# Optimization experiments

Measured on AMD Instinct MI355X. Metric: run time of the kernel, lower is better.

## Reference

```python
import jax, jax.numpy as jnp
import numpy as np

N = 50000       # nodes
D_IN = 256      # in_channels
D_OUT = 256     # out_channels
E1 = 300000     # edges for TAGConv branch
E2 = 300000     # edges for attention branch


def setup_inputs() -> dict:
    key = jax.random.key(0)
    ks = jax.random.split(key, 8)
    s = 1.0 / np.sqrt(D_IN)  # torch Linear default init range
    u = lambda k: jax.random.uniform(k, (D_IN, D_OUT), jnp.float32, -s, s)
    return {
        "x": jax.random.normal(ks[0], (N, D_IN), jnp.float32),
        "edge_index": jax.random.randint(ks[1], (2, E1), 0, N),
        "edge_index_2": jax.random.randint(ks[2], (2, E2), 0, N),
        "W0": u(ks[3]),  # TAGConv hop-0 weight
        "W1": u(ks[4]),  # TAGConv hop-1 weight
        "Wq": u(ks[5]),  # attention query proj
        "Wk": u(ks[6]),  # attention key proj
        "Wv": u(ks[7]),  # attention value proj
    }


def reference(x, edge_index, edge_index_2, W0, W1, Wq, Wk, Wv):
    # --- TAGConv branch: K=1, normalize=False, bias=False ---
    src, dst = edge_index[0], edge_index[1]
    agg = jax.ops.segment_sum(x[src], dst, num_segments=N)   # A @ x, [N, D_IN]
    x1 = x @ W0 + agg @ W1                                   # [N, D_OUT]

    # --- Transformer_Block branch over edge_index_2, use_softmax=False ---
    q = x @ Wq
    k = x @ Wk
    v = x @ Wv
    s2, d2 = edge_index_2[0], edge_index_2[1]
    attn = jnp.einsum('ed,ed->e', q[d2], k[s2])              # per-edge raw score
    x2 = jax.ops.segment_sum(attn[:, None] * v[s2], d2, num_segments=N)

    return x1 - x2
```

## Files before the change

### kernel.cpp

```cpp
#include <hip/hip_runtime.h>

#define TD 256

typedef __attribute__((ext_vector_type(8))) short short8;
typedef __attribute__((ext_vector_type(8))) unsigned short ushort8;
typedef __attribute__((ext_vector_type(4))) float f32x4;

__device__ inline unsigned short f2bf(float f) {
  unsigned u = __float_as_uint(f);
  u = u + 0x7fffu + ((u >> 16) & 1u);
  return (unsigned short)(u >> 16);
}
__device__ inline float bf2f(unsigned short h) {
  return __uint_as_float(((unsigned)h) << 16);
}

__global__ __launch_bounds__(256) void prologue_kernel(
    const int* __restrict__ ei, int E1, const int* __restrict__ ei2, int E2,
    int* __restrict__ deg1, int* __restrict__ deg2,
    const float* __restrict__ x, unsigned short* __restrict__ xb, long total8,
    const float* __restrict__ Wq, const float* __restrict__ Wk,
    unsigned short* __restrict__ wqb, unsigned short* __restrict__ wkb,
    const float* __restrict__ W0, const float* __restrict__ W1,
    const float* __restrict__ Wv, unsigned short* __restrict__ wt,
    int nbH, int nbX) {
  int b = blockIdx.x;
  if (b < nbH) {
    int stride = nbH * 256;
    int Emax = max(E1, E2);
    for (int i = b * 256 + threadIdx.x; i < Emax; i += stride) {
      if (i < E1) atomicAdd(&deg1[ei[E1 + i]], 1);
      if (i < E2) atomicAdd(&deg2[ei2[E2 + i]], 1);
    }
  } else if (b < nbH + nbX) {
    long t = (long)(b - nbH) * 256 + threadIdx.x;
    if (t >= total8) return;
    const float4 f0 = *reinterpret_cast<const float4*>(x + t * 8);
    const float4 f1 = *reinterpret_cast<const float4*>(x + t * 8 + 4);
    ushort8 o;
    o[0] = f2bf(f0.x); o[1] = f2bf(f0.y); o[2] = f2bf(f0.z); o[3] = f2bf(f0.w);
    o[4] = f2bf(f1.x); o[5] = f2bf(f1.y); o[6] = f2bf(f1.z); o[7] = f2bf(f1.w);
    *reinterpret_cast<ushort8*>(xb + t * 8) = o;
  } else if (b < nbH + nbX + 64) {
    int t = (b - nbH - nbX) * 256 + threadIdx.x;
    const float* src = (t < 8192) ? Wq : Wk;
    unsigned short* dst = (t < 8192) ? wqb : wkb;
    int o = (t & 8191) * 8;
    ushort8 r;
#pragma unroll
    for (int j = 0; j < 8; j++) r[j] = f2bf(src[o + j]);
    *reinterpret_cast<ushort8*>(dst + o) = r;
  } else {
    int b2 = b - nbH - nbX - 64;
    int m = b2 >> 8;
    int n = b2 & 255;
    int k = threadIdx.x;
    const float* W = m == 0 ? W0 : m == 1 ? W1 : Wv;
    wt[m * 65536 + n * 256 + k] = f2bf(W[k * 256 + n]);
  }
}

__global__ __launch_bounds__(256) void scanA_gemmG_kernel(
    const int* __restrict__ deg1, const int* __restrict__ deg2, int N,
    int* __restrict__ bsum,
    const unsigned short* __restrict__ wqb, const unsigned short* __restrict__ wkb,
    unsigned short* __restrict__ gt) {
  if (blockIdx.x < 512) {
    int arr = blockIdx.x >> 8;
    int b = blockIdx.x & 255;
    const int* deg = arr ? deg2 : deg1;
    int i = b * 256 + threadIdx.x;
    int v = (i < N) ? deg[i] : 0;
#pragma unroll
    for (int m = 1; m < 64; m <<= 1) v += __shfl_xor(v, m, 64);
    __shared__ int wsum[4];
    if ((threadIdx.x & 63) == 0) wsum[threadIdx.x >> 6] = v;
    __syncthreads();
    if (threadIdx.x == 0)
      bsum[blockIdx.x] = wsum[0] + wsum[1] + wsum[2] + wsum[3];
    return;
  }
  const int t = (blockIdx.x - 512) * 4 + (threadIdx.x >> 6);
  const int l = threadIdx.x & 63;
  const int a0 = (t >> 2) * 64;
  const int b0 = (t & 3) * 64;
  const int lc = l & 15;
  const int lk = l >> 4;
  f32x4 acc[4][4] = {};
#pragma unroll
  for (int ks = 0; ks < 256; ks += 32) {
    const int ko = ks + lk * 8;
    short8 a[4], b[4];
#pragma unroll
    for (int m = 0; m < 4; m++)
      a[m] = *reinterpret_cast<const short8*>(wqb + (a0 + m * 16 + lc) * 256 + ko);
#pragma unroll
    for (int n = 0; n < 4; n++)
      b[n] = *reinterpret_cast<const short8*>(wkb + (b0 + n * 16 + lc) * 256 + ko);
#pragma unroll
    for (int m = 0; m < 4; m++)
#pragma unroll
      for (int n = 0; n < 4; n++)
        acc[m][n] =
            __builtin_amdgcn_mfma_f32_16x16x32_bf16(a[m], b[n], acc[m][n], 0, 0, 0);
  }
#pragma unroll
  for (int m = 0; m < 4; m++)
#pragma unroll
    for (int n = 0; n < 4; n++)
#pragma unroll
      for (int j = 0; j < 4; j++) {
        int a = a0 + m * 16 + lk * 4 + j;
        int b = b0 + n * 16 + lc;
        gt[b * 256 + a] = f2bf(acc[m][n][j]);
      }
}

__global__ __launch_bounds__(256) void scan_fill_kernel(
    const int* __restrict__ deg1, const int* __restrict__ deg2,
    const int* __restrict__ bsum, int N,
    int* __restrict__ off1, int* __restrict__ cur1,
    int* __restrict__ off2, int* __restrict__ cur2) {
  int arr = blockIdx.x >> 8;
  int b = blockIdx.x & 255;
  const int* deg = arr ? deg2 : deg1;
  int* off = arr ? off2 : off1;
  int* cur = arr ? cur2 : cur1;
  const int t = threadIdx.x;

  __shared__ int redp[4], redt[4];
  int sval = bsum[arr * 256 + t];
  int pv = (t < b) ? sval : 0;
  int tv = sval;
#pragma unroll
  for (int m = 1; m < 64; m <<= 1) {
    pv += __shfl_xor(pv, m, 64);
    tv += __shfl_xor(tv, m, 64);
  }
  if ((t & 63) == 0) { redp[t >> 6] = pv; redt[t >> 6] = tv; }
  __syncthreads();
  int prefix = redp[0] + redp[1] + redp[2] + redp[3];
  int total = redt[0] + redt[1] + redt[2] + redt[3];
  if (b == 255 && t == 0) off[N] = total;

  int i = b * 256 + t;
  __shared__ int sm[256];
  int v = (i < N) ? deg[i] : 0;
  sm[t] = v;
  __syncthreads();
  for (int d = 1; d < 256; d <<= 1) {
    int val = (t >= d) ? sm[t - d] : 0;
    __syncthreads();
    sm[t] += val;
    __syncthreads();
  }
  int e = sm[t] - v + prefix;
  if (i < N) {
    off[i] = e;
    cur[i] = e;
  }
}

__global__ __launch_bounds__(256) void fill_kernel(
    const int* __restrict__ ei, int E1, const int* __restrict__ ei2, int E2,
    int* __restrict__ cur1, int* __restrict__ cur2,
    int* __restrict__ csr1, int* __restrict__ csr2) {
  int stride = gridDim.x * blockDim.x;
  int Emax = max(E1, E2);
  for (int i = blockIdx.x * blockDim.x + threadIdx.x; i < Emax; i += stride) {
    if (i < E1) {
      int d = ei[E1 + i];
      int p = atomicAdd(&cur1[d], 1);
      csr1[p] = ei[i];
    }
    if (i < E2) {
      int d = ei2[E2 + i];
      int p = atomicAdd(&cur2[d], 1);
      csr2[p] = ei2[i];
    }
  }
}

__global__ __launch_bounds__(256) void gather_fused_kernel(
    const unsigned short* __restrict__ xb, const unsigned short* __restrict__ qb,
    const int* __restrict__ off1, const int* __restrict__ csr1,
    const int* __restrict__ off2, const int* __restrict__ csr2,
    int N, unsigned short* __restrict__ aggb, unsigned short* __restrict__ tb) {
  int wid = blockIdx.x * 4 + (threadIdx.x >> 6);
  if (wid >= N) return;
  int lane = threadIdx.x & 63;

  {
    int beg = off1[wid], end = off1[wid + 1];
    float ax = 0.f, ay = 0.f, az = 0.f, aw = 0.f;
    for (int j = beg; j < end; j += 4) {
      int e1 = end - 1;
      int s0 = csr1[j];
      int s1 = csr1[j + 1 < end ? j + 1 : e1];
      int s2 = csr1[j + 2 < end ? j + 2 : e1];
      int s3 = csr1[j + 3 < end ? j + 3 : e1];
      float m1 = (j + 1 < end) ? 1.f : 0.f;
      float m2 = (j + 2 < end) ? 1.f : 0.f;
      float m3 = (j + 3 < end) ? 1.f : 0.f;
      ushort4 r0 = *reinterpret_cast<const ushort4*>(xb + (size_t)s0 * TD + lane * 4);
      ushort4 r1 = *reinterpret_cast<const ushort4*>(xb + (size_t)s1 * TD + lane * 4);
      ushort4 r2 = *reinterpret_cast<const ushort4*>(xb + (size_t)s2 * TD + lane * 4);
      ushort4 r3 = *reinterpret_cast<const ushort4*>(xb + (size_t)s3 * TD + lane * 4);
      ax += bf2f(r0.x) + m1 * bf2f(r1.x) + m2 * bf2f(r2.x) + m3 * bf2f(r3.x);
      ay += bf2f(r0.y) + m1 * bf2f(r1.y) + m2 * bf2f(r2.y) + m3 * bf2f(r3.y);
      az += bf2f(r0.z) + m1 * bf2f(r1.z) + m2 * bf2f(r2.z) + m3 * bf2f(r3.z);
      aw += bf2f(r0.w) + m1 * bf2f(r1.w) + m2 * bf2f(r2.w) + m3 * bf2f(r3.w);
    }
    ushort4 o;
    o.x = f2bf(ax); o.y = f2bf(ay); o.z = f2bf(az); o.w = f2bf(aw);
    *reinterpret_cast<ushort4*>(aggb + (size_t)wid * TD + lane * 4) = o;
  }

  {
    ushort4 qv = *reinterpret_cast<const ushort4*>(qb + (size_t)wid * TD + lane * 4);
    float qx = bf2f(qv.x), qy = bf2f(qv.y), qz = bf2f(qv.z), qw = bf2f(qv.w);
    int beg = off2[wid], end = off2[wid + 1];
    float tx = 0.f, ty = 0.f, tz = 0.f, tw = 0.f;
    for (int j = beg; j < end; j += 4) {
      int e1 = end - 1;
      int s0 = csr2[j];
      int s1 = csr2[j + 1 < end ? j + 1 : e1];
      int s2 = csr2[j + 2 < end ? j + 2 : e1];
      int s3 = csr2[j + 3 < end ? j + 3 : e1];
      ushort4 r0 = *reinterpret_cast<const ushort4*>(xb + (size_t)s0 * TD + lane * 4);
      ushort4 r1 = *reinterpret_cast<const ushort4*>(xb + (size_t)s1 * TD + lane * 4);
      ushort4 r2 = *reinterpret_cast<const ushort4*>(xb + (size_t)s2 * TD + lane * 4);
      ushort4 r3 = *reinterpret_cast<const ushort4*>(xb + (size_t)s3 * TD + lane * 4);
      float a0x = bf2f(r0.x), a0y = bf2f(r0.y), a0z = bf2f(r0.z), a0w = bf2f(r0.w);
      float a1x = bf2f(r1.x), a1y = bf2f(r1.y), a1z = bf2f(r1.z), a1w = bf2f(r1.w);
      float a2x = bf2f(r2.x), a2y = bf2f(r2.y), a2z = bf2f(r2.z), a2w = bf2f(r2.w);
      float a3x = bf2f(r3.x), a3y = bf2f(r3.y), a3z = bf2f(r3.z), a3w = bf2f(r3.w);
      float p0 = qx * a0x + qy * a0y + qz * a0z + qw * a0w;
      float p1 = qx * a1x + qy * a1y + qz * a1z + qw * a1w;
      float p2 = qx * a2x + qy * a2y + qz * a2z + qw * a2w;
      float p3 = qx * a3x + qy * a3y + qz * a3z + qw * a3w;
#pragma unroll
      for (int m = 1; m < 64; m <<= 1) {
        p0 += __shfl_xor(p0, m, 64);
        p1 += __shfl_xor(p1, m, 64);
        p2 += __shfl_xor(p2, m, 64);
        p3 += __shfl_xor(p3, m, 64);
      }
      p1 = (j + 1 < end) ? p1 : 0.f;
      p2 = (j + 2 < end) ? p2 : 0.f;
      p3 = (j + 3 < end) ? p3 : 0.f;
      tx -= p0 * a0x + p1 * a1x + p2 * a2x + p3 * a3x;
      ty -= p0 * a0y + p1 * a1y + p2 * a2y + p3 * a3y;
      tz -= p0 * a0z + p1 * a1z + p2 * a2z + p3 * a3z;
      tw -= p0 * a0w + p1 * a1w + p2 * a2w + p3 * a3w;
    }
    ushort4 o;
    o.x = f2bf(tx); o.y = f2bf(ty); o.z = f2bf(tz); o.w = f2bf(tw);
    *reinterpret_cast<ushort4*>(tb + (size_t)wid * TD + lane * 4) = o;
  }
}

template <int MODE>
__global__ __launch_bounds__(512) void gemm_lds(
    const unsigned short* __restrict__ xb, const unsigned short* __restrict__ aggb,
    const unsigned short* __restrict__ tb, const unsigned short* __restrict__ wt,
    const unsigned short* __restrict__ gt, float* __restrict__ out,
    unsigned short* __restrict__ qb, int M) {
  __shared__ __align__(16) unsigned short sA[128 * 64];
  __shared__ __align__(16) unsigned short sB[256 * 64];

  const int m0 = blockIdx.x * 128;
  const int tid = threadIdx.x;
  const int w = tid >> 6, l = tid & 63;
  const int lrow = l >> 3, lslot = l & 7;
  const int wr = w >> 2, wc = w & 3;

  f32x4 acc[4][4] = {};

  const int KTOT = (MODE == 0) ? 256 : 768;

  for (int k0 = 0; k0 < KTOT; k0 += 64) {
    const unsigned short* Ap;
    const unsigned short* Bp;
    int ks;
    if (MODE == 0) {
      Ap = xb; Bp = gt; ks = k0;
    } else {
      int seg = k0 >> 8;
      Ap = seg == 0 ? xb : seg == 1 ? aggb : tb;
      Bp = wt + seg * 65536;
      ks = k0 & 255;
    }

#pragma unroll
    for (int i = 0; i < 2; i++) {
      int row = w * 16 + i * 8 + lrow;
      int gr = m0 + row;
      if (gr >= M) gr = M - 1;
      int g = lslot ^ lrow;
      const unsigned short* src = Ap + (size_t)gr * TD + ks + g * 8;
      unsigned short* dst = sA + (w * 16 + i * 8) * 64;
      __builtin_amdgcn_global_load_lds(
          (const __attribute__((address_space(1))) void*)src,
          (__attribute__((address_space(3))) void*)dst, 16, 0, 0);
    }
#pragma unroll
    for (int i = 0; i < 4; i++) {
      int row = w * 32 + i * 8 + lrow;
      int g = lslot ^ lrow;
      const unsigned short* src = Bp + (size_t)row * TD + ks + g * 8;
      unsigned short* dst = sB + (w * 32 + i * 8) * 64;
      __builtin_amdgcn_global_load_lds(
          (const __attribute__((address_space(1))) void*)src,
          (__attribute__((address_space(3))) void*)dst, 16, 0, 0);
    }
    __syncthreads();

#pragma unroll
    for (int kk = 0; kk < 2; kk++) {
      short8 a[4], b[4];
#pragma unroll
      for (int m = 0; m < 4; m++) {
        int row = wr * 64 + m * 16 + (l & 15);
        int slot = (kk * 4 + (l >> 4)) ^ (row & 7);
        a[m] = *reinterpret_cast<const short8*>(&sA[row * 64 + slot * 8]);
      }
#pragma unroll
      for (int n = 0; n < 4; n++) {
        int row = wc * 64 + n * 16 + (l & 15);
        int slot = (kk * 4 + (l >> 4)) ^ (row & 7);
        b[n] = *reinterpret_cast<const short8*>(&sB[row * 64 + slot * 8]);
      }
#pragma unroll
      for (int m = 0; m < 4; m++)
#pragma unroll
        for (int n = 0; n < 4; n++)
          acc[m][n] =
              __builtin_amdgcn_mfma_f32_16x16x32_bf16(a[m], b[n], acc[m][n], 0, 0, 0);
    }
    __syncthreads();
  }

  if (MODE == 1) {
#pragma unroll
    for (int m = 0; m < 4; m++)
#pragma unroll
      for (int n = 0; n < 4; n++)
#pragma unroll
        for (int j = 0; j < 4; j++) {
          int r = m0 + wr * 64 + m * 16 + (l >> 4) * 4 + j;
          if (r < M)
            out[(size_t)r * TD + wc * 64 + n * 16 + (l & 15)] = acc[m][n][j];
        }
  } else {
#pragma unroll
    for (int m = 0; m < 4; m++)
#pragma unroll
      for (int n = 0; n < 4; n++)
#pragma unroll
        for (int j = 0; j < 4; j++) {
          int r = m0 + wr * 64 + m * 16 + (l >> 4) * 4 + j;
          if (r < M)
            qb[(size_t)r * TD + wc * 64 + n * 16 + (l & 15)] =
                f2bf(acc[m][n][j]);
        }
  }
}

extern "C" void kernel_launch(void* const* d_in, const int* in_sizes, int n_in,
                              void* d_out, int out_size, void* d_ws,
                              size_t ws_size, hipStream_t stream) {
  const float* x  = (const float*)d_in[0];
  const int*   ei  = (const int*)d_in[1];
  const int*   ei2 = (const int*)d_in[2];
  const float* W0 = (const float*)d_in[3];
  const float* W1 = (const float*)d_in[4];
  const float* Wq = (const float*)d_in[5];
  const float* Wk = (const float*)d_in[6];
  const float* Wv = (const float*)d_in[7];

  const int N  = in_sizes[0] / TD;
  const int E1 = in_sizes[1] / 2;
  const int E2 = in_sizes[2] / 2;

  float* out = (float*)d_out;
  const size_t rowN = (size_t)N * TD;

  char* p = (char*)d_ws;
  unsigned short* xb   = (unsigned short*)p; p += rowN * 2;
  unsigned short* aggb = (unsigned short*)p; p += rowN * 2;
  unsigned short* qb   = (unsigned short*)p; p += rowN * 2;
  unsigned short* tb   = (unsigned short*)p; p += rowN * 2;
  unsigned short* wt   = (unsigned short*)p; p += 3 * 65536 * 2;
  unsigned short* gt   = (unsigned short*)p; p += 65536 * 2;
  unsigned short* wqb  = (unsigned short*)p; p += 65536 * 2;
  unsigned short* wkb  = (unsigned short*)p; p += 65536 * 2;
  int* off1 = (int*)p; p += (N + 1) * 4;
  int* cur1 = (int*)p; p += N * 4;
  int* off2 = (int*)p; p += (N + 1) * 4;
  int* cur2 = (int*)p; p += N * 4;
  int* csr1 = (int*)p; p += (size_t)E1 * 4;
  int* csr2 = (int*)p; p += (size_t)E2 * 4;
  int* deg1 = (int*)p; p += N * 4;
  int* deg2 = (int*)p; p += N * 4;
  int* bsum = (int*)p; p += 512 * 4;

  hipMemsetAsync(deg1, 0, (size_t)2 * N * sizeof(int), stream);

  long total8 = rowN / 8;
  int nbH = 512;
  int nbX = (int)((total8 + 255) / 256);
  prologue_kernel<<<nbH + nbX + 64 + 768, 256, 0, stream>>>(
      ei, E1, ei2, E2, deg1, deg2, x, xb, total8, Wq, Wk, wqb, wkb, W0, W1, Wv,
      wt, nbH, nbX);

  scanA_gemmG_kernel<<<516, 256, 0, stream>>>(deg1, deg2, N, bsum, wqb, wkb, gt);
  scan_fill_kernel<<<512, 256, 0, stream>>>(deg1, deg2, bsum, N, off1, cur1,
                                            off2, cur2);
  fill_kernel<<<1024, 256, 0, stream>>>(ei, E1, ei2, E2, cur1, cur2, csr1, csr2);

  int gblk = (N + 127) / 128;
  gemm_lds<0><<<gblk, 512, 0, stream>>>(xb, aggb, tb, wt, gt, out, qb, N);

  gather_fused_kernel<<<(N + 3) / 4, 256, 0, stream>>>(xb, qb, off1, csr1,
                                                       off2, csr2, N, aggb, tb);

  gemm_lds<1><<<gblk, 512, 0, stream>>>(xb, aggb, tb, wt, gt, out, qb, N);
}
```

Before: 183.0 us.

## Merge CSR fill into q-GEMM launch and widen gather to 16-byte loads

```diff
diff --git a/kernel.cpp b/kernel.cpp
--- a/kernel.cpp
+++ b/kernel.cpp
@@ -161,115 +161,34 @@
   }
 }
 
-__global__ __launch_bounds__(256) void fill_kernel(
+__global__ __launch_bounds__(512) void fill_gemm0_kernel(
     const int* __restrict__ ei, int E1, const int* __restrict__ ei2, int E2,
     int* __restrict__ cur1, int* __restrict__ cur2,
-    int* __restrict__ csr1, int* __restrict__ csr2) {
-  int stride = gridDim.x * blockDim.x;
-  int Emax = max(E1, E2);
-  for (int i = blockIdx.x * blockDim.x + threadIdx.x; i < Emax; i += stride) {
-    if (i < E1) {
-      int d = ei[E1 + i];
-      int p = atomicAdd(&cur1[d], 1);
-      csr1[p] = ei[i];
-    }
-    if (i < E2) {
-      int d = ei2[E2 + i];
-      int p = atomicAdd(&cur2[d], 1);
-      csr2[p] = ei2[i];
-    }
-  }
-}
-
-__global__ __launch_bounds__(256) void gather_fused_kernel(
-    const unsigned short* __restrict__ xb, const unsigned short* __restrict__ qb,
-    const int* __restrict__ off1, const int* __restrict__ csr1,
-    const int* __restrict__ off2, const int* __restrict__ csr2,
-    int N, unsigned short* __restrict__ aggb, unsigned short* __restrict__ tb) {
-  int wid = blockIdx.x * 4 + (threadIdx.x >> 6);
-  if (wid >= N) return;
-  int lane = threadIdx.x & 63;
-
-  {
-    int beg = off1[wid], end = off1[wid + 1];
-    float ax = 0.f, ay = 0.f, az = 0.f, aw = 0.f;
-    for (int j = beg; j < end; j += 4) {
-      int e1 = end - 1;
-      int s0 = csr1[j];
-      int s1 = csr1[j + 1 < end ? j + 1 : e1];
-      int s2 = csr1[j + 2 < end ? j + 2 : e1];
-      int s3 = csr1[j + 3 < end ? j + 3 : e1];
-      float m1 = (j + 1 < end) ? 1.f : 0.f;
-      float m2 = (j + 2 < end) ? 1.f : 0.f;
-      float m3 = (j + 3 < end) ? 1.f : 0.f;
-      ushort4 r0 = *reinterpret_cast<const ushort4*>(xb + (size_t)s0 * TD + lane * 4);
-      ushort4 r1 = *reinterpret_cast<const ushort4*>(xb + (size_t)s1 * TD + lane * 4);
-      ushort4 r2 = *reinterpret_cast<const ushort4*>(xb + (size_t)s2 * TD + lane * 4);
-      ushort4 r3 = *reinterpret_cast<const ushort4*>(xb + (size_t)s3 * TD + lane * 4);
-      ax += bf2f(r0.x) + m1 * bf2f(r1.x) + m2 * bf2f(r2.x) + m3 * bf2f(r3.x);
-      ay += bf2f(r0.y) + m1 * bf2f(r1.y) + m2 * bf2f(r2.y) + m3 * bf2f(r3.y);
-      az += bf2f(r0.z) + m1 * bf2f(r1.z) + m2 * bf2f(r2.z) + m3 * bf2f(r3.z);
-      aw += bf2f(r0.w) + m1 * bf2f(r1.w) + m2 * bf2f(r2.w) + m3 * bf2f(r3.w);
-    }
-    ushort4 o;
-    o.x = f2bf(ax); o.y = f2bf(ay); o.z = f2bf(az); o.w = f2bf(aw);
-    *reinterpret_cast<ushort4*>(aggb + (size_t)wid * TD + lane * 4) = o;
-  }
-
-  {
-    ushort4 qv = *reinterpret_cast<const ushort4*>(qb + (size_t)wid * TD + lane * 4);
-    float qx = bf2f(qv.x), qy = bf2f(qv.y), qz = bf2f(qv.z), qw = bf2f(qv.w);
-    int beg = off2[wid], end = off2[wid + 1];
-    float tx = 0.f, ty = 0.f, tz = 0.f, tw = 0.f;
-    for (int j = beg; j < end; j += 4) {
-      int e1 = end - 1;
-      int s0 = csr2[j];
-      int s1 = csr2[j + 1 < end ? j + 1 : e1];
-      int s2 = csr2[j + 2 < end ? j + 2 : e1];
-      int s3 = csr2[j + 3 < end ? j + 3 : e1];
-      ushort4 r0 = *reinterpret_cast<const ushort4*>(xb + (size_t)s0 * TD + lane * 4);
-      ushort4 r1 = *reinterpret_cast<const ushort4*>(xb + (size_t)s1 * TD + lane * 4);
-      ushort4 r2 = *reinterpret_cast<const ushort4*>(xb + (size_t)s2 * TD + lane * 4);
-      ushort4 r3 = *reinterpret_cast<const ushort4*>(xb + (size_t)s3 * TD + lane * 4);
-      float a0x = bf2f(r0.x), a0y = bf2f(r0.y), a0z = bf2f(r0.z), a0w = bf2f(r0.w);
-      float a1x = bf2f(r1.x), a1y = bf2f(r1.y), a1z = bf2f(r1.z), a1w = bf2f(r1.w);
-      float a2x = bf2f(r2.x), a2y = bf2f(r2.y), a2z = bf2f(r2.z), a2w = bf2f(r2.w);
-      float a3x = bf2f(r3.x), a3y = bf2f(r3.y), a3z = bf2f(r3.z), a3w = bf2f(r3.w);
-      float p0 = qx * a0x + qy * a0y + qz * a0z + qw * a0w;
-      float p1 = qx * a1x + qy * a1y + qz * a1z + qw * a1w;
-      float p2 = qx * a2x + qy * a2y + qz * a2z + qw * a2w;
-      float p3 = qx * a3x + qy * a3y + qz * a3z + qw * a3w;
-#pragma unroll
-      for (int m = 1; m < 64; m <<= 1) {
-        p0 += __shfl_xor(p0, m, 64);
-        p1 += __shfl_xor(p1, m, 64);
-        p2 += __shfl_xor(p2, m, 64);
-        p3 += __shfl_xor(p3, m, 64);
-      }
-      p1 = (j + 1 < end) ? p1 : 0.f;
-      p2 = (j + 2 < end) ? p2 : 0.f;
-      p3 = (j + 3 < end) ? p3 : 0.f;
-      tx -= p0 * a0x + p1 * a1x + p2 * a2x + p3 * a3x;
-      ty -= p0 * a0y + p1 * a1y + p2 * a2y + p3 * a3y;
-      tz -= p0 * a0z + p1 * a1z + p2 * a2z + p3 * a3z;
-      tw -= p0 * a0w + p1 * a1w + p2 * a2w + p3 * a3w;
-    }
-    ushort4 o;
-    o.x = f2bf(tx); o.y = f2bf(ty); o.z = f2bf(tz); o.w = f2bf(tw);
-    *reinterpret_cast<ushort4*>(tb + (size_t)wid * TD + lane * 4) = o;
-  }
-}
-
-template <int MODE>
-__global__ __launch_bounds__(512) void gemm_lds(
-    const unsigned short* __restrict__ xb, const unsigned short* __restrict__ aggb,
-    const unsigned short* __restrict__ tb, const unsigned short* __restrict__ wt,
-    const unsigned short* __restrict__ gt, float* __restrict__ out,
-    unsigned short* __restrict__ qb, int M) {
+    int* __restrict__ csr1, int* __restrict__ csr2,
+    const unsigned short* __restrict__ xb, const unsigned short* __restrict__ gt,
+    unsigned short* __restrict__ qb, int M, int FB) {
   __shared__ __align__(16) unsigned short sA[128 * 64];
   __shared__ __align__(16) unsigned short sB[256 * 64];
 
-  const int m0 = blockIdx.x * 128;
+  if (blockIdx.x < FB) {
+    int stride = FB * 512;
+    int Emax = max(E1, E2);
+    for (int i = blockIdx.x * 512 + threadIdx.x; i < Emax; i += stride) {
+      if (i < E1) {
+        int d = ei[E1 + i];
+        int p = atomicAdd(&cur1[d], 1);
+        csr1[p] = ei[i];
+      }
+      if (i < E2) {
+        int d = ei2[E2 + i];
+        int p = atomicAdd(&cur2[d], 1);
+        csr2[p] = ei2[i];
+      }
+    }
+    return;
+  }
+
+  const int m0 = (blockIdx.x - FB) * 128;
   const int tid = threadIdx.x;
   const int w = tid >> 6, l = tid & 63;
   const int lrow = l >> 3, lslot = l & 7;
@@ -277,20 +196,10 @@
 
   f32x4 acc[4][4] = {};
 
-  const int KTOT = (MODE == 0) ? 256 : 768;
-
-  for (int k0 = 0; k0 < KTOT; k0 += 64) {
-    const unsigned short* Ap;
-    const unsigned short* Bp;
-    int ks;
-    if (MODE == 0) {
-      Ap = xb; Bp = gt; ks = k0;
-    } else {
-      int seg = k0 >> 8;
-      Ap = seg == 0 ? xb : seg == 1 ? aggb : tb;
-      Bp = wt + seg * 65536;
-      ks = k0 & 255;
-    }
+  for (int k0 = 0; k0 < 256; k0 += 64) {
+    const unsigned short* Ap = xb;
+    const unsigned short* Bp = gt;
+    int ks = k0;
 
 #pragma unroll
     for (int i = 0; i < 2; i++) {
@@ -341,30 +250,178 @@
     __syncthreads();
   }
 
-  if (MODE == 1) {
-#pragma unroll
-    for (int m = 0; m < 4; m++)
-#pragma unroll
-      for (int n = 0; n < 4; n++)
-#pragma unroll
-        for (int j = 0; j < 4; j++) {
-          int r = m0 + wr * 64 + m * 16 + (l >> 4) * 4 + j;
-          if (r < M)
-            out[(size_t)r * TD + wc * 64 + n * 16 + (l & 15)] = acc[m][n][j];
-        }
-  } else {
-#pragma unroll
-    for (int m = 0; m < 4; m++)
-#pragma unroll
-      for (int n = 0; n < 4; n++)
-#pragma unroll
-        for (int j = 0; j < 4; j++) {
-          int r = m0 + wr * 64 + m * 16 + (l >> 4) * 4 + j;
-          if (r < M)
-            qb[(size_t)r * TD + wc * 64 + n * 16 + (l & 15)] =
-                f2bf(acc[m][n][j]);
-        }
-  }
+#pragma unroll
+  for (int m = 0; m < 4; m++)
+#pragma unroll
+    for (int n = 0; n < 4; n++)
+#pragma unroll
+      for (int j = 0; j < 4; j++) {
+        int r = m0 + wr * 64 + m * 16 + (l >> 4) * 4 + j;
+        if (r < M)
+          qb[(size_t)r * TD + wc * 64 + n * 16 + (l & 15)] = f2bf(acc[m][n][j]);
+      }
+}
+
+__global__ __launch_bounds__(256) void gather_fused_kernel(
+    const unsigned short* __restrict__ xb, const unsigned short* __restrict__ qb,
+    const int* __restrict__ off1, const int* __restrict__ csr1,
+    const int* __restrict__ off2, const int* __restrict__ csr2,
+    int N, unsigned short* __restrict__ aggb, unsigned short* __restrict__ tb) {
+  int wid = blockIdx.x * 4 + (threadIdx.x >> 6);
+  if (wid >= N) return;
+  const int lane = threadIdx.x & 63;
+  const int eh = lane >> 5;
+  const int sl = lane & 31;
+
+  {
+    int beg = off1[wid], end = off1[wid + 1];
+    float acc[8] = {};
+    for (int j = beg; j < end; j += 4) {
+      int e1 = end - 1;
+      int j0 = j + eh, j1 = j + 2 + eh;
+      int s0 = csr1[j0 < end ? j0 : e1];
+      int s1 = csr1[j1 < end ? j1 : e1];
+      float k0 = (j0 < end) ? 1.f : 0.f;
+      float k1 = (j1 < end) ? 1.f : 0.f;
+      ushort8 r0 = *reinterpret_cast<const ushort8*>(xb + (size_t)s0 * TD + sl * 8);
+      ushort8 r1 = *reinterpret_cast<const ushort8*>(xb + (size_t)s1 * TD + sl * 8);
+#pragma unroll
+      for (int i = 0; i < 8; i++)
+        acc[i] += k0 * bf2f(r0[i]) + k1 * bf2f(r1[i]);
+    }
+#pragma unroll
+    for (int i = 0; i < 8; i++) acc[i] += __shfl_xor(acc[i], 32, 64);
+    if (eh == 0) {
+      ushort8 o;
+#pragma unroll
+      for (int i = 0; i < 8; i++) o[i] = f2bf(acc[i]);
+      *reinterpret_cast<ushort8*>(aggb + (size_t)wid * TD + sl * 8) = o;
+    }
+  }
+
+  {
+    ushort8 qv = *reinterpret_cast<const ushort8*>(qb + (size_t)wid * TD + sl * 8);
+    float q[8];
+#pragma unroll
+    for (int i = 0; i < 8; i++) q[i] = bf2f(qv[i]);
+    int beg = off2[wid], end = off2[wid + 1];
+    float t[8] = {};
+    for (int j = beg; j < end; j += 4) {
+      int e1 = end - 1;
+      int j0 = j + eh, j1 = j + 2 + eh;
+      int s0 = csr2[j0 < end ? j0 : e1];
+      int s1 = csr2[j1 < end ? j1 : e1];
+      float k0 = (j0 < end) ? 1.f : 0.f;
+      float k1 = (j1 < end) ? 1.f : 0.f;
+      ushort8 r0 = *reinterpret_cast<const ushort8*>(xb + (size_t)s0 * TD + sl * 8);
+      ushort8 r1 = *reinterpret_cast<const ushort8*>(xb + (size_t)s1 * TD + sl * 8);
+      float x0[8], x1[8];
+      float p0 = 0.f, p1 = 0.f;
+#pragma unroll
+      for (int i = 0; i < 8; i++) {
+        x0[i] = bf2f(r0[i]); x1[i] = bf2f(r1[i]);
+        p0 += q[i] * x0[i];  p1 += q[i] * x1[i];
+      }
+#pragma unroll
+      for (int m = 1; m < 32; m <<= 1) {
+        p0 += __shfl_xor(p0, m, 64);
+        p1 += __shfl_xor(p1, m, 64);
+      }
+      p0 *= k0; p1 *= k1;
+#pragma unroll
+      for (int i = 0; i < 8; i++) t[i] -= p0 * x0[i] + p1 * x1[i];
+    }
+#pragma unroll
+    for (int i = 0; i < 8; i++) t[i] += __shfl_xor(t[i], 32, 64);
+    if (eh == 0) {
+      ushort8 o;
+#pragma unroll
+      for (int i = 0; i < 8; i++) o[i] = f2bf(t[i]);
+      *reinterpret_cast<ushort8*>(tb + (size_t)wid * TD + sl * 8) = o;
+    }
+  }
+}
+
+__global__ __launch_bounds__(512) void gemm1_kernel(
+    const unsigned short* __restrict__ xb, const unsigned short* __restrict__ aggb,
+    const unsigned short* __restrict__ tb, const unsigned short* __restrict__ wt,
+    float* __restrict__ out, int M) {
+  __shared__ __align__(16) unsigned short sA[128 * 64];
+  __shared__ __align__(16) unsigned short sB[256 * 64];
+
+  const int m0 = blockIdx.x * 128;
+  const int tid = threadIdx.x;
+  const int w = tid >> 6, l = tid & 63;
+  const int lrow = l >> 3, lslot = l & 7;
+  const int wr = w >> 2, wc = w & 3;
+
+  f32x4 acc[4][4] = {};
+
+  for (int k0 = 0; k0 < 768; k0 += 64) {
+    int seg = k0 >> 8;
+    const unsigned short* Ap = seg == 0 ? xb : seg == 1 ? aggb : tb;
+    const unsigned short* Bp = wt + seg * 65536;
+    int ks = k0 & 255;
+
+#pragma unroll
+    for (int i = 0; i < 2; i++) {
+      int row = w * 16 + i * 8 + lrow;
+      int gr = m0 + row;
+      if (gr >= M) gr = M - 1;
+      int g = lslot ^ lrow;
+      const unsigned short* src = Ap + (size_t)gr * TD + ks + g * 8;
+      unsigned short* dst = sA + (w * 16 + i * 8) * 64;
+      __builtin_amdgcn_global_load_lds(
+          (const __attribute__((address_space(1))) void*)src,
+          (__attribute__((address_space(3))) void*)dst, 16, 0, 0);
+    }
+#pragma unroll
+    for (int i = 0; i < 4; i++) {
+      int row = w * 32 + i * 8 + lrow;
+      int g = lslot ^ lrow;
+      const unsigned short* src = Bp + (size_t)row * TD + ks + g * 8;
+      unsigned short* dst = sB + (w * 32 + i * 8) * 64;
+      __builtin_amdgcn_global_load_lds(
+          (const __attribute__((address_space(1))) void*)src,
+          (__attribute__((address_space(3))) void*)dst, 16, 0, 0);
+    }
+    __syncthreads();
+
+#pragma unroll
+    for (int kk = 0; kk < 2; kk++) {
+      short8 a[4], b[4];
+#pragma unroll
+      for (int m = 0; m < 4; m++) {
+        int row = wr * 64 + m * 16 + (l & 15);
+        int slot = (kk * 4 + (l >> 4)) ^ (row & 7);
+        a[m] = *reinterpret_cast<const short8*>(&sA[row * 64 + slot * 8]);
+      }
+#pragma unroll
+      for (int n = 0; n < 4; n++) {
+        int row = wc * 64 + n * 16 + (l & 15);
+        int slot = (kk * 4 + (l >> 4)) ^ (row & 7);
+        b[n] = *reinterpret_cast<const short8*>(&sB[row * 64 + slot * 8]);
+      }
+#pragma unroll
+      for (int m = 0; m < 4; m++)
+#pragma unroll
+        for (int n = 0; n < 4; n++)
+          acc[m][n] =
+              __builtin_amdgcn_mfma_f32_16x16x32_bf16(a[m], b[n], acc[m][n], 0, 0, 0);
+    }
+    __syncthreads();
+  }
+
+#pragma unroll
+  for (int m = 0; m < 4; m++)
+#pragma unroll
+    for (int n = 0; n < 4; n++)
+#pragma unroll
+      for (int j = 0; j < 4; j++) {
+        int r = m0 + wr * 64 + m * 16 + (l >> 4) * 4 + j;
+        if (r < M)
+          out[(size_t)r * TD + wc * 64 + n * 16 + (l & 15)] = acc[m][n][j];
+      }
 }
 
 extern "C" void kernel_launch(void* const* d_in, const int* in_sizes, int n_in,
@@ -417,13 +474,14 @@
   scanA_gemmG_kernel<<<516, 256, 0, stream>>>(deg1, deg2, N, bsum, wqb, wkb, gt);
   scan_fill_kernel<<<512, 256, 0, stream>>>(deg1, deg2, bsum, N, off1, cur1,
                                             off2, cur2);
-  fill_kernel<<<1024, 256, 0, stream>>>(ei, E1, ei2, E2, cur1, cur2, csr1, csr2);
 
   int gblk = (N + 127) / 128;
-  gemm_lds<0><<<gblk, 512, 0, stream>>>(xb, aggb, tb, wt, gt, out, qb, N);
+  int FB = 384;
+  fill_gemm0_kernel<<<FB + gblk, 512, 0, stream>>>(
+      ei, E1, ei2, E2, cur1, cur2, csr1, csr2, xb, gt, qb, N, FB);
 
   gather_fused_kernel<<<(N + 3) / 4, 256, 0, stream>>>(xb, qb, off1, csr1,
                                                        off2, csr2, N, aggb, tb);
 
-  gemm_lds<1><<<gblk, 512, 0, stream>>>(xb, aggb, tb, wt, gt, out, qb, N);
-}
+  gemm1_kernel<<<gblk, 512, 0, stream>>>(xb, aggb, tb, wt, out, N);
+}
```

Measured after the change: 178.2 us (median of 2 runs). -2.6%, faster.
